# Optimization experiments

Measured on AMD Instinct MI355X. Metric: run time of the kernel, lower is better.

The kernel has to match this reference:

```python
import jax, jax.numpy as jnp
import numpy as np

B, N, L, K, C1 = 128, 300, 600, 19, 100  # batch, num_cnns, input_length, filter_size, fc hidden
PS = 7  # pool size == stride
LC = L - (K - 1)               # 582, conv output length
LP = (LC - PS) // PS + 1       # 83, pooled length
NC = 2                         # num_classes
EPS = 1e-5


def _bn(x, g, b, m, v):
    # eval-mode batchnorm, params broadcast along given axes already
    return g * (x - m) * jax.lax.rsqrt(v + EPS) + b


def setup_inputs() -> dict:
    key = jax.random.key(0)
    ks = jax.random.split(key, 20)
    f = lambda i, shape, s=0.1: (jax.random.normal(ks[i], shape, dtype=jnp.float32) * s)
    pv = lambda i, shape: (jax.random.uniform(ks[i], shape, dtype=jnp.float32) + 0.5)
    return {
        'x': jax.random.normal(ks[0], (B, 4, L), dtype=jnp.float32),
        'conv_w': f(1, (N, 4, K)), 'conv_b': f(2, (N,)),
        'bn1_g': pv(3, (N,)), 'bn1_b': f(4, (N,)), 'bn1_m': f(5, (N,)), 'bn1_v': pv(6, (N,)),
        'fc1_w': f(7, (N, C1, LP)), 'fc1_b': f(8, (N, C1)),
        'bn2_g': pv(9, (N, C1)), 'bn2_b': f(10, (N, C1)), 'bn2_m': f(11, (N, C1)), 'bn2_v': pv(12, (N, C1)),
        'fc2_w': f(13, (N, C1)), 'fc2_b': f(14, (N,)),
        'bn3_g': pv(15, (N,)), 'bn3_b': f(16, (N,)), 'bn3_m': f(17, (N,)), 'bn3_v': pv(18, (N,)),
        'final_w': f(19, (NC, N)), 'final_b': jnp.zeros((NC,), dtype=jnp.float32),
    }


def reference(x, conv_w, conv_b, bn1_g, bn1_b, bn1_m, bn1_v,
              fc1_w, fc1_b, bn2_g, bn2_b, bn2_m, bn2_v,
              fc2_w, fc2_b, bn3_g, bn3_b, bn3_m, bn3_v,
              final_w, final_b):
    # grouped conv on a repeated input == plain conv with 4 in-channels, N out-channels
    h = jax.lax.conv_general_dilated(x, conv_w, window_strides=(1,), padding='VALID',
                                     dimension_numbers=('NCH', 'OIH', 'NCH'))  # [B,N,582]
    h = h + conv_b[None, :, None]
    h = _bn(h, bn1_g[None, :, None], bn1_b[None, :, None], bn1_m[None, :, None], bn1_v[None, :, None])
    h = jnp.exp(h)
    # MaxPool1d(7,7): [B,N,582] -> [B,N,83]
    h = jax.lax.reduce_window(h, -jnp.inf, jax.lax.max,
                              window_dimensions=(1, 1, PS), window_strides=(1, 1, PS), padding='VALID')
    # grouped 1x1 conv == per-unit dense: [B,N,83] x [N,100,83] -> [B,N,100]
    h = jnp.einsum('bnp,nhp->bnh', h, fc1_w) + fc1_b[None]
    h = jax.nn.relu(_bn(h, bn2_g[None], bn2_b[None], bn2_m[None], bn2_v[None]))
    # second grouped 1x1 conv: [B,N,100] x [N,100] -> [B,N]
    h = jnp.einsum('bnh,nh->bn', h, fc2_w) + fc2_b[None]
    h = jax.nn.relu(_bn(h, bn3_g[None], bn3_b[None], bn3_m[None], bn3_v[None]))
    return h @ final_w.T + final_b  # [B,num_classes]
```

## Files before the change

kernel.cpp:

```cpp
#include <hip/hip_runtime.h>
#include <math.h>

#define EPS_ 1e-5f

__global__ __launch_bounds__(256) void kA(
        const float* __restrict__ x,
        const float* __restrict__ conv_w,
        const float* __restrict__ conv_b,
        const float* __restrict__ g1, const float* __restrict__ b1,
        const float* __restrict__ m1, const float* __restrict__ v1,
        float* __restrict__ pooled)
{
    __shared__ float xs[4 * 600];
    __shared__ float sw[3 * 76];
    __shared__ float sA[3], sB[3];
    const int tid = threadIdx.x;
    const int b   = blockIdx.y;
    const int n0  = blockIdx.x * 3;

    for (int i = tid; i < 4 * 600; i += 256) xs[i] = x[b * 2400 + i];
    for (int i = tid; i < 3 * 76;  i += 256) sw[i] = conv_w[n0 * 76 + i];
    if (tid < 3) {
        const int n = n0 + tid;
        const float A = g1[n] * rsqrtf(v1[n] + EPS_);
        sA[tid] = A;
        sB[tid] = A * (conv_b[n] - m1[n]) + b1[n];
    }
    __syncthreads();

    if (tid < 249) {
        const int nl = tid / 83;
        const int p  = tid % 83;
        const int base = 7 * p;
        float acc[7];
        #pragma unroll
        for (int q = 0; q < 7; ++q) acc[q] = 0.f;

        #pragma unroll
        for (int c = 0; c < 4; ++c) {
            float xv[25];
            #pragma unroll
            for (int d = 0; d < 25; ++d) xv[d] = xs[c * 600 + base + d];
            #pragma unroll
            for (int k = 0; k < 19; ++k) {
                const float wv = sw[nl * 76 + c * 19 + k];
                #pragma unroll
                for (int q = 0; q < 7; ++q)
                    acc[q] = fmaf(xv[q + k], wv, acc[q]);
            }
        }
        const float A = sA[nl], Bc = sB[nl];
        float mx = -INFINITY;
        #pragma unroll
        for (int q = 0; q < 7; ++q) mx = fmaxf(mx, fmaf(A, acc[q], Bc));
        const int n = n0 + nl;
        pooled[(size_t)n * (128 * 83) + b * 83 + p] = __expf(mx);
    }
}

__global__ __launch_bounds__(256) void kB(
        const float* __restrict__ pooled,
        const float* __restrict__ fc1_w,
        const float* __restrict__ fc1_b,
        const float* __restrict__ g2, const float* __restrict__ b2,
        const float* __restrict__ m2, const float* __restrict__ v2,
        const float* __restrict__ fc2_w,
        const float* __restrict__ fc2_b,
        const float* __restrict__ g3, const float* __restrict__ b3,
        const float* __restrict__ m3, const float* __restrict__ v3,
        float* __restrict__ sout)
{
    __shared__ float sW[100 * 83];
    __shared__ float sP[16 * 83];
    __shared__ float sAct[16 * 100];
    __shared__ float sw2[100];
    __shared__ float sA2[100], sC2[100];
    const int tid = threadIdx.x;
    const int n   = blockIdx.y;
    const int b0  = blockIdx.x * 16;

    for (int i = tid; i < 100 * 83; i += 256) sW[i] = fc1_w[(size_t)n * 8300 + i];
    for (int i = tid; i < 16 * 83;  i += 256)
        sP[i] = pooled[(size_t)n * (128 * 83) + b0 * 83 + i];
    if (tid < 100) {
        const int i = n * 100 + tid;
        const float A = g2[i] * rsqrtf(v2[i] + EPS_);
        sA2[tid] = A;
        sC2[tid] = A * (fc1_b[i] - m2[i]) + b2[i];
        sw2[tid] = fc2_w[i];
    }
    __syncthreads();

    const int bl = tid & 15;
    const int hi = tid >> 4;
    for (int hb = 0; hb < 7; ++hb) {
        const int h = hb * 16 + hi;
        if (h < 100) {
            float dot = 0.f;
            for (int p = 0; p < 83; ++p)
                dot = fmaf(sW[h * 83 + p], sP[bl * 83 + p], dot);
            const float z = fmaf(sA2[h], dot, sC2[h]);
            sAct[bl * 100 + h] = fmaxf(z, 0.f);
        }
    }
    __syncthreads();

    const int g = tid >> 4, j = tid & 15;
    float acc = 0.f;
    for (int h = j; h < 100; h += 16) acc += sAct[g * 100 + h] * sw2[h];
    #pragma unroll
    for (int off = 8; off > 0; off >>= 1) acc += __shfl_xor(acc, off, 16);
    if (j == 0) {
        const float val = acc + fc2_b[n];
        const float A3 = g3[n] * rsqrtf(v3[n] + EPS_);
        const float z = A3 * (val - m3[n]) + b3[n];
        sout[(size_t)(b0 + g) * 300 + n] = fmaxf(z, 0.f);
    }
}

__global__ __launch_bounds__(64) void kC(
        const float* __restrict__ sout,
        const float* __restrict__ fw,
        const float* __restrict__ fb,
        float* __restrict__ out)
{
    const int b = blockIdx.x, t = threadIdx.x;
    float a0 = 0.f, a1 = 0.f;
    for (int nn = t; nn < 300; nn += 64) {
        const float v = sout[b * 300 + nn];
        a0 = fmaf(v, fw[nn], a0);
        a1 = fmaf(v, fw[300 + nn], a1);
    }
    #pragma unroll
    for (int off = 32; off > 0; off >>= 1) {
        a0 += __shfl_xor(a0, off, 64);
        a1 += __shfl_xor(a1, off, 64);
    }
    if (t == 0) {
        out[b * 2 + 0] = a0 + fb[0];
        out[b * 2 + 1] = a1 + fb[1];
    }
}

extern "C" void kernel_launch(void* const* d_in, const int* in_sizes, int n_in,
                              void* d_out, int out_size, void* d_ws, size_t ws_size,
                              hipStream_t stream) {
    const float* x      = (const float*)d_in[0];
    const float* conv_w = (const float*)d_in[1];
    const float* conv_b = (const float*)d_in[2];
    const float* g1 = (const float*)d_in[3];
    const float* b1 = (const float*)d_in[4];
    const float* m1 = (const float*)d_in[5];
    const float* v1 = (const float*)d_in[6];
    const float* fc1_w = (const float*)d_in[7];
    const float* fc1_b = (const float*)d_in[8];
    const float* g2 = (const float*)d_in[9];
    const float* b2 = (const float*)d_in[10];
    const float* m2 = (const float*)d_in[11];
    const float* v2 = (const float*)d_in[12];
    const float* fc2_w = (const float*)d_in[13];
    const float* fc2_b = (const float*)d_in[14];
    const float* g3 = (const float*)d_in[15];
    const float* b3 = (const float*)d_in[16];
    const float* m3 = (const float*)d_in[17];
    const float* v3 = (const float*)d_in[18];
    const float* fw = (const float*)d_in[19];
    const float* fb = (const float*)d_in[20];
    float* out = (float*)d_out;

    float* pooled = (float*)d_ws;
    float* sout   = pooled + (size_t)300 * 128 * 83;

    kA<<<dim3(100, 128), 256, 0, stream>>>(x, conv_w, conv_b, g1, b1, m1, v1, pooled);
    kB<<<dim3(8, 300), 256, 0, stream>>>(pooled, fc1_w, fc1_b, g2, b2, m2, v2,
                                         fc2_w, fc2_b, g3, b3, m3, v3, sout);
    kC<<<128, 64, 0, stream>>>(sout, fw, fb, out);
}
```

Baseline: 202.1 us.

## Register-tile conv over 3 filters per thread and fc1 as 4x7 micro-GEMM

```diff
diff --git a/kernel.cpp b/kernel.cpp
--- a/kernel.cpp
+++ b/kernel.cpp
@@ -11,20 +11,29 @@
         const float* __restrict__ m1, const float* __restrict__ v1,
         float* __restrict__ pooled)
 {
-    __shared__ float xs[4 * 600];
-    __shared__ float sw[3 * 76];
-    __shared__ float sA[3], sB[3];
+    __shared__ __align__(16) float xs[4 * 600];
+    __shared__ float sw[9 * 76];
+    __shared__ float sA[9], sB[9];
     const int tid = threadIdx.x;
     const int b   = blockIdx.y;
-    const int n0  = blockIdx.x * 3;
-
-    for (int i = tid; i < 4 * 600; i += 256) xs[i] = x[b * 2400 + i];
-    for (int i = tid; i < 3 * 76;  i += 256) sw[i] = conv_w[n0 * 76 + i];
-    if (tid < 3) {
+    const int n0  = blockIdx.x * 9;
+
+    {
+        const float4* src = reinterpret_cast<const float4*>(x + (size_t)b * 2400);
+        float4* dst = reinterpret_cast<float4*>(xs);
+        for (int i = tid; i < 600; i += 256) dst[i] = src[i];
+    }
+    for (int i = tid; i < 9 * 76; i += 256) {
+        const int gi = n0 * 76 + i;
+        sw[i] = (gi < 300 * 76) ? conv_w[gi] : 0.f;
+    }
+    if (tid < 9) {
         const int n = n0 + tid;
-        const float A = g1[n] * rsqrtf(v1[n] + EPS_);
-        sA[tid] = A;
-        sB[tid] = A * (conv_b[n] - m1[n]) + b1[n];
+        if (n < 300) {
+            const float A = g1[n] * rsqrtf(v1[n] + EPS_);
+            sA[tid] = A;
+            sB[tid] = A * (conv_b[n] - m1[n]) + b1[n];
+        } else { sA[tid] = 0.f; sB[tid] = 0.f; }
     }
     __syncthreads();
 
@@ -32,29 +41,47 @@
         const int nl = tid / 83;
         const int p  = tid % 83;
         const int base = 7 * p;
-        float acc[7];
-        #pragma unroll
-        for (int q = 0; q < 7; ++q) acc[q] = 0.f;
-
-        #pragma unroll
+        float acc[3][7];
+        #pragma unroll
+        for (int m = 0; m < 3; ++m)
+            #pragma unroll
+            for (int q = 0; q < 7; ++q) acc[m][q] = 0.f;
+
         for (int c = 0; c < 4; ++c) {
-            float xv[25];
-            #pragma unroll
-            for (int d = 0; d < 25; ++d) xv[d] = xs[c * 600 + base + d];
+            const float* xc = &xs[c * 600 + base];
+            const float* wc = &sw[nl * 3 * 76 + c * 19];
+            float win[7];
+            #pragma unroll
+            for (int j = 0; j < 7; ++j) win[j] = xc[j];
             #pragma unroll
             for (int k = 0; k < 19; ++k) {
-                const float wv = sw[nl * 76 + c * 19 + k];
+                const float w0 = wc[k];
+                const float w1 = wc[76 + k];
+                const float w2 = wc[152 + k];
                 #pragma unroll
-                for (int q = 0; q < 7; ++q)
-                    acc[q] = fmaf(xv[q + k], wv, acc[q]);
+                for (int q = 0; q < 7; ++q) {
+                    acc[0][q] = fmaf(win[q], w0, acc[0][q]);
+                    acc[1][q] = fmaf(win[q], w1, acc[1][q]);
+                    acc[2][q] = fmaf(win[q], w2, acc[2][q]);
+                }
+                if (k < 18) {
+                    #pragma unroll
+                    for (int j = 0; j < 6; ++j) win[j] = win[j + 1];
+                    win[6] = xc[k + 7];
+                }
             }
         }
-        const float A = sA[nl], Bc = sB[nl];
-        float mx = -INFINITY;
-        #pragma unroll
-        for (int q = 0; q < 7; ++q) mx = fmaxf(mx, fmaf(A, acc[q], Bc));
-        const int n = n0 + nl;
-        pooled[(size_t)n * (128 * 83) + b * 83 + p] = __expf(mx);
+        #pragma unroll
+        for (int m = 0; m < 3; ++m) {
+            const int n = n0 + nl * 3 + m;
+            if (n < 300) {
+                const float A = sA[nl * 3 + m], Bc = sB[nl * 3 + m];
+                float mx = -INFINITY;
+                #pragma unroll
+                for (int q = 0; q < 7; ++q) mx = fmaxf(mx, fmaf(A, acc[m][q], Bc));
+                pooled[(size_t)n * (128 * 83) + b * 83 + p] = __expf(mx);
+            }
+        }
     }
 }
 
@@ -70,51 +97,83 @@
         const float* __restrict__ m3, const float* __restrict__ v3,
         float* __restrict__ sout)
 {
-    __shared__ float sW[100 * 83];
-    __shared__ float sP[16 * 83];
-    __shared__ float sAct[16 * 100];
-    __shared__ float sw2[100];
-    __shared__ float sA2[100], sC2[100];
+    __shared__ __align__(16) float sW[112 * 84];
+    __shared__ __align__(16) float sP[64 * 84];
+    __shared__ float sRed[16][64];
+    __shared__ float sA2[112], sC2[112], sw2[112];
     const int tid = threadIdx.x;
     const int n   = blockIdx.y;
-    const int b0  = blockIdx.x * 16;
-
-    for (int i = tid; i < 100 * 83; i += 256) sW[i] = fc1_w[(size_t)n * 8300 + i];
-    for (int i = tid; i < 16 * 83;  i += 256)
-        sP[i] = pooled[(size_t)n * (128 * 83) + b0 * 83 + i];
-    if (tid < 100) {
-        const int i = n * 100 + tid;
-        const float A = g2[i] * rsqrtf(v2[i] + EPS_);
-        sA2[tid] = A;
-        sC2[tid] = A * (fc1_b[i] - m2[i]) + b2[i];
-        sw2[tid] = fc2_w[i];
+    const int b0  = blockIdx.x * 64;
+
+    for (int i = tid; i < 112 * 84; i += 256) {
+        const int h = i / 84, k = i - h * 84;
+        sW[i] = (h < 100 && k < 83) ? fc1_w[(size_t)n * 8300 + h * 83 + k] : 0.f;
+    }
+    for (int i = tid; i < 64 * 84; i += 256) {
+        const int bl = i / 84, p = i - bl * 84;
+        sP[i] = (p < 83) ? pooled[(size_t)n * (128 * 83) + (b0 + bl) * 83 + p] : 0.f;
+    }
+    if (tid < 112) {
+        if (tid < 100) {
+            const int i = n * 100 + tid;
+            const float A = g2[i] * rsqrtf(v2[i] + EPS_);
+            sA2[tid] = A;
+            sC2[tid] = A * (fc1_b[i] - m2[i]) + b2[i];
+            sw2[tid] = fc2_w[i];
+        } else { sA2[tid] = 0.f; sC2[tid] = 0.f; sw2[tid] = 0.f; }
     }
     __syncthreads();
 
-    const int bl = tid & 15;
-    const int hi = tid >> 4;
-    for (int hb = 0; hb < 7; ++hb) {
-        const int h = hb * 16 + hi;
-        if (h < 100) {
-            float dot = 0.f;
-            for (int p = 0; p < 83; ++p)
-                dot = fmaf(sW[h * 83 + p], sP[bl * 83 + p], dot);
-            const float z = fmaf(sA2[h], dot, sC2[h]);
-            sAct[bl * 100 + h] = fmaxf(z, 0.f);
+    const int bg = tid >> 4;
+    const int hg = tid & 15;
+    float acc[4][7];
+    #pragma unroll
+    for (int i = 0; i < 4; ++i)
+        #pragma unroll
+        for (int j = 0; j < 7; ++j) acc[i][j] = 0.f;
+
+    for (int k0 = 0; k0 < 84; k0 += 4) {
+        float4 wv[7], pv[4];
+        #pragma unroll
+        for (int j = 0; j < 7; ++j)
+            wv[j] = *reinterpret_cast<const float4*>(&sW[(hg * 7 + j) * 84 + k0]);
+        #pragma unroll
+        for (int i = 0; i < 4; ++i)
+            pv[i] = *reinterpret_cast<const float4*>(&sP[(bg * 4 + i) * 84 + k0]);
+        #pragma unroll
+        for (int i = 0; i < 4; ++i)
+            #pragma unroll
+            for (int j = 0; j < 7; ++j) {
+                acc[i][j] = fmaf(pv[i].x, wv[j].x, acc[i][j]);
+                acc[i][j] = fmaf(pv[i].y, wv[j].y, acc[i][j]);
+                acc[i][j] = fmaf(pv[i].z, wv[j].z, acc[i][j]);
+                acc[i][j] = fmaf(pv[i].w, wv[j].w, acc[i][j]);
+            }
+    }
+
+    float part[4] = {0.f, 0.f, 0.f, 0.f};
+    #pragma unroll
+    for (int j = 0; j < 7; ++j) {
+        const int h = hg * 7 + j;
+        const float a2 = sA2[h], c2 = sC2[h], w2 = sw2[h];
+        #pragma unroll
+        for (int i = 0; i < 4; ++i) {
+            const float z = fmaxf(fmaf(a2, acc[i][j], c2), 0.f);
+            part[i] = fmaf(z, w2, part[i]);
         }
     }
+    #pragma unroll
+    for (int i = 0; i < 4; ++i) sRed[hg][bg * 4 + i] = part[i];
     __syncthreads();
 
-    const int g = tid >> 4, j = tid & 15;
-    float acc = 0.f;
-    for (int h = j; h < 100; h += 16) acc += sAct[g * 100 + h] * sw2[h];
-    #pragma unroll
-    for (int off = 8; off > 0; off >>= 1) acc += __shfl_xor(acc, off, 16);
-    if (j == 0) {
-        const float val = acc + fc2_b[n];
+    if (tid < 64) {
+        float s = 0.f;
+        #pragma unroll
+        for (int g = 0; g < 16; ++g) s += sRed[g][tid];
+        s += fc2_b[n];
         const float A3 = g3[n] * rsqrtf(v3[n] + EPS_);
-        const float z = A3 * (val - m3[n]) + b3[n];
-        sout[(size_t)(b0 + g) * 300 + n] = fmaxf(z, 0.f);
+        const float z = A3 * (s - m3[n]) + b3[n];
+        sout[(size_t)(b0 + tid) * 300 + n] = fmaxf(z, 0.f);
     }
 }
 
@@ -171,8 +230,8 @@
     float* pooled = (float*)d_ws;
     float* sout   = pooled + (size_t)300 * 128 * 83;
 
-    kA<<<dim3(100, 128), 256, 0, stream>>>(x, conv_w, conv_b, g1, b1, m1, v1, pooled);
-    kB<<<dim3(8, 300), 256, 0, stream>>>(pooled, fc1_w, fc1_b, g2, b2, m2, v2,
+    kA<<<dim3(34, 128), 256, 0, stream>>>(x, conv_w, conv_b, g1, b1, m1, v1, pooled);
+    kB<<<dim3(2, 300), 256, 0, stream>>>(pooled, fc1_w, fc1_b, g2, b2, m2, v2,
                                          fc2_w, fc2_b, g3, b3, m3, v3, sout);
     kC<<<128, 64, 0, stream>>>(sout, fw, fb, out);
 }
```

After: 201.6 us. Within noise of the previous version (-0.2%).

## Transpose input batch-innermost and restructure conv and FC stages around wavefront-uniform weights

Applied to the files above, without the earlier changes.

```diff
diff --git a/kernel.cpp b/kernel.cpp
--- a/kernel.cpp
+++ b/kernel.cpp
@@ -3,118 +3,177 @@
 
 #define EPS_ 1e-5f
 
-__global__ __launch_bounds__(256) void kA(
-        const float* __restrict__ x,
+__device__ __forceinline__ float rfl(float v) {
+    return __int_as_float(__builtin_amdgcn_readfirstlane(__float_as_int(v)));
+}
+
+__global__ __launch_bounds__(256) void kT(const float* __restrict__ x,
+                                          float* __restrict__ xT) {
+    __shared__ float sX[128 * 25];
+    const int tid = threadIdx.x;
+    const int t0  = blockIdx.x * 20;
+    const int c   = blockIdx.y;
+    for (int i = tid; i < 128 * 5; i += 256) {
+        const int b = i / 5, f = i % 5;
+        const float4 v = *reinterpret_cast<const float4*>(
+            x + b * 2400 + c * 600 + t0 + 4 * f);
+        sX[b * 25 + 4 * f + 0] = v.x;
+        sX[b * 25 + 4 * f + 1] = v.y;
+        sX[b * 25 + 4 * f + 2] = v.z;
+        sX[b * 25 + 4 * f + 3] = v.w;
+    }
+    __syncthreads();
+    for (int j = tid; j < 20 * 128; j += 256) {
+        const int tt = j >> 7, b = j & 127;
+        xT[(c * 600 + t0 + tt) * 128 + b] = sX[b * 25 + tt];
+    }
+}
+
+__global__ __launch_bounds__(64, 3) void kA(
+        const float* __restrict__ xT,
         const float* __restrict__ conv_w,
         const float* __restrict__ conv_b,
         const float* __restrict__ g1, const float* __restrict__ b1,
         const float* __restrict__ m1, const float* __restrict__ v1,
         float* __restrict__ pooled)
 {
-    __shared__ float xs[4 * 600];
-    __shared__ float sw[3 * 76];
-    __shared__ float sA[3], sB[3];
-    const int tid = threadIdx.x;
-    const int b   = blockIdx.y;
-    const int n0  = blockIdx.x * 3;
-
-    for (int i = tid; i < 4 * 600; i += 256) xs[i] = x[b * 2400 + i];
-    for (int i = tid; i < 3 * 76;  i += 256) sw[i] = conv_w[n0 * 76 + i];
-    if (tid < 3) {
-        const int n = n0 + tid;
-        const float A = g1[n] * rsqrtf(v1[n] + EPS_);
-        sA[tid] = A;
-        sB[tid] = A * (conv_b[n] - m1[n]) + b1[n];
-    }
-    __syncthreads();
-
-    if (tid < 249) {
-        const int nl = tid / 83;
-        const int p  = tid % 83;
-        const int base = 7 * p;
+    const int wid = blockIdx.x;
+    const int n   = wid >> 3;
+    const int r   = wid & 7;
+    const int bh  = r >> 2;
+    const int pr  = r & 3;
+    const int p0  = pr * 21;
+    const int np  = (pr < 3) ? 21 : 20;
+    const int bb  = bh * 64 + threadIdx.x;
+
+    float w[4][19];
+    #pragma unroll
+    for (int c = 0; c < 4; ++c)
+        #pragma unroll
+        for (int k = 0; k < 19; ++k)
+            w[c][k] = rfl(conv_w[n * 76 + c * 19 + k]);
+
+    const float A1 = rfl(g1[n]) * rsqrtf(rfl(v1[n]) + EPS_);
+    const float B1 = A1 * (rfl(conv_b[n]) - rfl(m1[n])) + rfl(b1[n]);
+
+    const float* xb = xT + bb;
+    float win[4][25];
+    {
+        const float* px = xb + (7 * p0) * 128;
+        #pragma unroll
+        for (int c = 0; c < 4; ++c)
+            #pragma unroll
+            for (int j = 0; j < 18; ++j)
+                win[c][j] = px[(c * 600 + j) * 128];
+    }
+
+    float* outp = pooled + (n * 83 + p0) * 128 + bb;
+    for (int p = 0; p < np; ++p) {
+        const float* px = xb + 7 * (p0 + p) * 128;
+        #pragma unroll
+        for (int c = 0; c < 4; ++c)
+            #pragma unroll
+            for (int j = 18; j < 25; ++j)
+                win[c][j] = px[(c * 600 + j) * 128];
+
         float acc[7];
         #pragma unroll
         for (int q = 0; q < 7; ++q) acc[q] = 0.f;
-
-        #pragma unroll
-        for (int c = 0; c < 4; ++c) {
-            float xv[25];
-            #pragma unroll
-            for (int d = 0; d < 25; ++d) xv[d] = xs[c * 600 + base + d];
+        #pragma unroll
+        for (int c = 0; c < 4; ++c)
             #pragma unroll
             for (int k = 0; k < 19; ++k) {
-                const float wv = sw[nl * 76 + c * 19 + k];
+                const float wv = w[c][k];
                 #pragma unroll
                 for (int q = 0; q < 7; ++q)
-                    acc[q] = fmaf(xv[q + k], wv, acc[q]);
+                    acc[q] = fmaf(win[c][k + q], wv, acc[q]);
             }
-        }
-        const float A = sA[nl], Bc = sB[nl];
         float mx = -INFINITY;
         #pragma unroll
-        for (int q = 0; q < 7; ++q) mx = fmaxf(mx, fmaf(A, acc[q], Bc));
-        const int n = n0 + nl;
-        pooled[(size_t)n * (128 * 83) + b * 83 + p] = __expf(mx);
+        for (int q = 0; q < 7; ++q) mx = fmaxf(mx, fmaf(A1, acc[q], B1));
+        outp[p * 128] = __expf(mx);
+
+        #pragma unroll
+        for (int c = 0; c < 4; ++c)
+            #pragma unroll
+            for (int j = 0; j < 18; ++j)
+                win[c][j] = win[c][j + 7];
     }
 }
 
 __global__ __launch_bounds__(256) void kB(
         const float* __restrict__ pooled,
-        const float* __restrict__ fc1_w,
-        const float* __restrict__ fc1_b,
+        const float* __restrict__ fc1w,
+        const float* __restrict__ fc1b,
         const float* __restrict__ g2, const float* __restrict__ b2,
         const float* __restrict__ m2, const float* __restrict__ v2,
-        const float* __restrict__ fc2_w,
-        const float* __restrict__ fc2_b,
+        const float* __restrict__ fc2w,
+        const float* __restrict__ fc2b,
         const float* __restrict__ g3, const float* __restrict__ b3,
         const float* __restrict__ m3, const float* __restrict__ v3,
         float* __restrict__ sout)
 {
-    __shared__ float sW[100 * 83];
-    __shared__ float sP[16 * 83];
-    __shared__ float sAct[16 * 100];
-    __shared__ float sw2[100];
-    __shared__ float sA2[100], sC2[100];
-    const int tid = threadIdx.x;
-    const int n   = blockIdx.y;
-    const int b0  = blockIdx.x * 16;
-
-    for (int i = tid; i < 100 * 83; i += 256) sW[i] = fc1_w[(size_t)n * 8300 + i];
-    for (int i = tid; i < 16 * 83;  i += 256)
-        sP[i] = pooled[(size_t)n * (128 * 83) + b0 * 83 + i];
-    if (tid < 100) {
-        const int i = n * 100 + tid;
-        const float A = g2[i] * rsqrtf(v2[i] + EPS_);
-        sA2[tid] = A;
-        sC2[tid] = A * (fc1_b[i] - m2[i]) + b2[i];
-        sw2[tid] = fc2_w[i];
-    }
+    __shared__ float sRed[4][64];
+    const int blk  = blockIdx.x;
+    const int n    = blk >> 1;
+    const int bh   = blk & 1;
+    const int tid  = threadIdx.x;
+    const int lane = tid & 63;
+    const int hg   = __builtin_amdgcn_readfirstlane(tid >> 6);
+    const int h0   = hg * 25;
+    const int bb   = bh * 64 + lane;
+
+    const float* pvb  = pooled + (n * 83) * 128 + bb;
+    const float* wrow = fc1w + (size_t)n * 8300 + h0 * 83;
+
+    float acc[25];
+    #pragma unroll
+    for (int j = 0; j < 25; ++j) acc[j] = 0.f;
+
+    for (int k0 = 0; k0 < 80; k0 += 16) {
+        float pv[16];
+        #pragma unroll
+        for (int kk = 0; kk < 16; ++kk) pv[kk] = pvb[(k0 + kk) * 128];
+        #pragma unroll
+        for (int j = 0; j < 25; ++j) {
+            #pragma unroll
+            for (int kk = 0; kk < 16; ++kk) {
+                const float wv = rfl(wrow[j * 83 + k0 + kk]);
+                acc[j] = fmaf(pv[kk], wv, acc[j]);
+            }
+        }
+    }
+    {
+        float pv[3];
+        #pragma unroll
+        for (int kk = 0; kk < 3; ++kk) pv[kk] = pvb[(80 + kk) * 128];
+        #pragma unroll
+        for (int j = 0; j < 25; ++j) {
+            #pragma unroll
+            for (int kk = 0; kk < 3; ++kk) {
+                const float wv = rfl(wrow[j * 83 + 80 + kk]);
+                acc[j] = fmaf(pv[kk], wv, acc[j]);
+            }
+        }
+    }
+
+    float part = 0.f;
+    #pragma unroll
+    for (int j = 0; j < 25; ++j) {
+        const int i = n * 100 + h0 + j;
+        const float A2 = rfl(g2[i]) * rsqrtf(rfl(v2[i]) + EPS_);
+        const float C2 = fmaf(A2, rfl(fc1b[i]) - rfl(m2[i]), rfl(b2[i]));
+        const float act = fmaxf(fmaf(A2, acc[j], C2), 0.f);
+        part = fmaf(act, rfl(fc2w[i]), part);
+    }
+    sRed[hg][lane] = part;
     __syncthreads();
-
-    const int bl = tid & 15;
-    const int hi = tid >> 4;
-    for (int hb = 0; hb < 7; ++hb) {
-        const int h = hb * 16 + hi;
-        if (h < 100) {
-            float dot = 0.f;
-            for (int p = 0; p < 83; ++p)
-                dot = fmaf(sW[h * 83 + p], sP[bl * 83 + p], dot);
-            const float z = fmaf(sA2[h], dot, sC2[h]);
-            sAct[bl * 100 + h] = fmaxf(z, 0.f);
-        }
-    }
-    __syncthreads();
-
-    const int g = tid >> 4, j = tid & 15;
-    float acc = 0.f;
-    for (int h = j; h < 100; h += 16) acc += sAct[g * 100 + h] * sw2[h];
-    #pragma unroll
-    for (int off = 8; off > 0; off >>= 1) acc += __shfl_xor(acc, off, 16);
-    if (j == 0) {
-        const float val = acc + fc2_b[n];
+    if (tid < 64) {
+        float s = sRed[0][lane] + sRed[1][lane] + sRed[2][lane] + sRed[3][lane];
+        s += fc2b[n];
         const float A3 = g3[n] * rsqrtf(v3[n] + EPS_);
-        const float z = A3 * (val - m3[n]) + b3[n];
-        sout[(size_t)(b0 + g) * 300 + n] = fmaxf(z, 0.f);
+        const float z = fmaf(A3, s - m3[n], b3[n]);
+        sout[n * 128 + bb] = fmaxf(z, 0.f);
     }
 }
 
@@ -127,7 +186,7 @@
     const int b = blockIdx.x, t = threadIdx.x;
     float a0 = 0.f, a1 = 0.f;
     for (int nn = t; nn < 300; nn += 64) {
-        const float v = sout[b * 300 + nn];
+        const float v = sout[nn * 128 + b];
         a0 = fmaf(v, fw[nn], a0);
         a1 = fmaf(v, fw[300 + nn], a1);
     }
@@ -168,11 +227,13 @@
     const float* fb = (const float*)d_in[20];
     float* out = (float*)d_out;
 
-    float* pooled = (float*)d_ws;
-    float* sout   = pooled + (size_t)300 * 128 * 83;
-
-    kA<<<dim3(100, 128), 256, 0, stream>>>(x, conv_w, conv_b, g1, b1, m1, v1, pooled);
-    kB<<<dim3(8, 300), 256, 0, stream>>>(pooled, fc1_w, fc1_b, g2, b2, m2, v2,
-                                         fc2_w, fc2_b, g3, b3, m3, v3, sout);
+    float* xT     = (float*)d_ws;
+    float* pooled = xT + 307200;
+    float* sout   = pooled + (size_t)300 * 83 * 128;
+
+    kT<<<dim3(30, 4), 256, 0, stream>>>(x, xT);
+    kA<<<2400, 64, 0, stream>>>(xT, conv_w, conv_b, g1, b1, m1, v1, pooled);
+    kB<<<600, 256, 0, stream>>>(pooled, fc1_w, fc1_b, g2, b2, m2, v2,
+                                fc2_w, fc2_b, g3, b3, m3, v3, sout);
     kC<<<128, 64, 0, stream>>>(sout, fw, fb, out);
 }
```

Measured after the change: 234.3 us. 15.9% more time.
